# Kernel optimization log

Measured on AMD Instinct MI355X. Metric: run time of the kernel, lower is better.

Reference implementation:

```python
import jax, jax.numpy as jnp
import numpy as np

N_NODES = 50000
N_EDGES = 800000
D = 64


def setup_inputs() -> dict:
    key = jax.random.key(0)
    ks = jax.random.split(key, 5)
    edge_feat = jax.random.normal(ks[0], (N_EDGES, D), dtype=jnp.float32)
    src = jax.random.randint(ks[1], (N_EDGES,), 0, N_NODES, dtype=jnp.int64)
    dst = jax.random.randint(ks[2], (N_EDGES,), 0, N_NODES, dtype=jnp.int64)
    W1 = jax.random.normal(ks[3], (D, D), dtype=jnp.float32) * (1.0 / np.sqrt(D))
    b1 = jnp.zeros((D,), dtype=jnp.float32)
    W2 = jax.random.normal(ks[4], (D, D), dtype=jnp.float32) * (1.0 / np.sqrt(D))
    b2 = jnp.zeros((D,), dtype=jnp.float32)
    return {"edge_feat": edge_feat, "src": src, "dst": dst,
            "W1": W1, "b1": b1, "W2": W2, "b2": b2}


def reference(edge_feat, src, dst, W1, b1, W2, b2):
    # update_all(copy_e, mailbox.sum): node x[v] = sum of edge_feat over edges with dst==v
    node_x = jax.ops.segment_sum(edge_feat, dst, num_segments=N_NODES)  # [N, D]
    # apply_edges: 0.5 * MLP(src.x + dst.x)
    inp = node_x[src] + node_x[dst]                                     # [E, D]
    h = jax.nn.relu(inp @ W1 + b1)
    edge_out = 0.5 * (h @ W2 + b2)                                      # [E, D]
    return edge_out
```

## Files before the change

kernel.cpp:

```cpp
#include <hip/hip_runtime.h>

#define NN 50000
#define NE 800000
#define DD 64
#define NB 196
#define EB 64

__global__ __launch_bounds__(256) void k_hist(const int* __restrict__ dst,
                                              int* __restrict__ cnt) {
    int e = blockIdx.x * 256 + threadIdx.x;
    if (e < NE) atomicAdd(&cnt[dst[e]], 1);
}

__global__ __launch_bounds__(256) void k_block_sum(const int* __restrict__ cnt,
                                                   int* __restrict__ bsum) {
    __shared__ int s[256];
    int i = blockIdx.x * 256 + threadIdx.x;
    s[threadIdx.x] = (i < NN) ? cnt[i] : 0;
    __syncthreads();
    for (int o = 128; o > 0; o >>= 1) {
        if (threadIdx.x < o) s[threadIdx.x] += s[threadIdx.x + o];
        __syncthreads();
    }
    if (threadIdx.x == 0) bsum[blockIdx.x] = s[0];
}

__global__ __launch_bounds__(256) void k_scan_bsum(int* __restrict__ bsum) {
    __shared__ int s[256];
    int t = threadIdx.x;
    int v = (t < NB) ? bsum[t] : 0;
    s[t] = v;
    __syncthreads();
    for (int o = 1; o < 256; o <<= 1) {
        int x = (t >= o) ? s[t - o] : 0;
        __syncthreads();
        s[t] += x;
        __syncthreads();
    }
    if (t < NB) bsum[t] = s[t] - v;
}

__global__ __launch_bounds__(256) void k_scan_final(const int* __restrict__ cnt,
                                                    const int* __restrict__ bsum,
                                                    int* __restrict__ row_start,
                                                    int* __restrict__ cursor) {
    __shared__ int s[256];
    int t = threadIdx.x;
    int i = blockIdx.x * 256 + t;
    int v = (i < NN) ? cnt[i] : 0;
    s[t] = v;
    __syncthreads();
    for (int o = 1; o < 256; o <<= 1) {
        int x = (t >= o) ? s[t - o] : 0;
        __syncthreads();
        s[t] += x;
        __syncthreads();
    }
    int excl = s[t] - v + bsum[blockIdx.x];
    if (i < NN) {
        row_start[i] = excl;
        cursor[i]    = excl;
        if (i == NN - 1) row_start[NN] = excl + v;
    }
}

__global__ __launch_bounds__(256) void k_reorder(const int* __restrict__ dst,
                                                 int* __restrict__ cursor,
                                                 int* __restrict__ eid) {
    int e = blockIdx.x * 256 + threadIdx.x;
    if (e < NE) {
        int pos = atomicAdd(&cursor[dst[e]], 1);
        eid[pos] = e;
    }
}

__global__ __launch_bounds__(256) void k_gather(const float* __restrict__ ef,
                                                const int* __restrict__ row_start,
                                                const int* __restrict__ eid,
                                                float* __restrict__ nx) {
    int lane = threadIdx.x & 63;
    int n = blockIdx.x * 4 + (threadIdx.x >> 6);
    if (n >= NN) return;
    int beg = row_start[n], end = row_start[n + 1];
    float a0 = 0.f, a1 = 0.f, a2 = 0.f, a3 = 0.f;
    int i = beg;
    for (; i + 3 < end; i += 4) {
        int e0 = eid[i], e1 = eid[i + 1], e2 = eid[i + 2], e3 = eid[i + 3];
        a0 += ef[(long)e0 * DD + lane];
        a1 += ef[(long)e1 * DD + lane];
        a2 += ef[(long)e2 * DD + lane];
        a3 += ef[(long)e3 * DD + lane];
    }
    for (; i < end; ++i) {
        a0 += ef[(long)eid[i] * DD + lane];
    }
    nx[(long)n * DD + lane] = (a0 + a1) + (a2 + a3);
}

#define ZERO4 make_float4(0.f, 0.f, 0.f, 0.f)

#define OP16(hv, wv)                                              \
    C0.x = fmaf(hv.x, wv.x, C0.x); C0.y = fmaf(hv.x, wv.y, C0.y); \
    C0.z = fmaf(hv.x, wv.z, C0.z); C0.w = fmaf(hv.x, wv.w, C0.w); \
    C1.x = fmaf(hv.y, wv.x, C1.x); C1.y = fmaf(hv.y, wv.y, C1.y); \
    C1.z = fmaf(hv.y, wv.z, C1.z); C1.w = fmaf(hv.y, wv.w, C1.w); \
    C2.x = fmaf(hv.z, wv.x, C2.x); C2.y = fmaf(hv.z, wv.y, C2.y); \
    C2.z = fmaf(hv.z, wv.z, C2.z); C2.w = fmaf(hv.z, wv.w, C2.w); \
    C3.x = fmaf(hv.w, wv.x, C3.x); C3.y = fmaf(hv.w, wv.y, C3.y); \
    C3.z = fmaf(hv.w, wv.z, C3.z); C3.w = fmaf(hv.w, wv.w, C3.w);

__global__ __launch_bounds__(256, 4) void k_node_mlp(const float* __restrict__ nx,
                                                     const float* __restrict__ W1,
                                                     float* __restrict__ hp) {
    __shared__ float sXT[DD][EB];
    __shared__ float4 sW[DD * DD / 4];
    const float4* Wv = (const float4*)W1;
#pragma unroll
    for (int i = 0; i < 4; ++i)
        sW[threadIdx.x + 256 * i] = Wv[threadIdx.x + 256 * i];

    int lane = threadIdx.x & 63;
    int w    = threadIdx.x >> 6;
    long n   = (long)blockIdx.x * EB + lane;
    const float4* px = (const float4*)(nx + n * DD) + 4 * w;
#pragma unroll
    for (int i = 0; i < 4; ++i) {
        float4 a = (n < NN) ? px[i] : ZERO4;
        int k = 16 * w + 4 * i;
        sXT[k + 0][lane] = a.x;
        sXT[k + 1][lane] = a.y;
        sXT[k + 2][lane] = a.z;
        sXT[k + 3][lane] = a.w;
    }
    __syncthreads();

    int tx = threadIdx.x & 15, ty = threadIdx.x >> 4;
    float4 C0 = ZERO4, C1 = ZERO4, C2 = ZERO4, C3 = ZERO4;
#pragma unroll 4
    for (int k = 0; k < DD; ++k) {
        float4 hv = *(const float4*)&sXT[k][4 * ty];
        float4 wv = sW[k * 16 + tx];
        OP16(hv, wv)
    }
    long r0 = (long)blockIdx.x * EB + 4 * ty;
    if (r0 + 0 < NN) ((float4*)(hp + (r0 + 0) * DD))[tx] = C0;
    if (r0 + 1 < NN) ((float4*)(hp + (r0 + 1) * DD))[tx] = C1;
    if (r0 + 2 < NN) ((float4*)(hp + (r0 + 2) * DD))[tx] = C2;
    if (r0 + 3 < NN) ((float4*)(hp + (r0 + 3) * DD))[tx] = C3;
}

__global__ __launch_bounds__(256, 4) void k_edge_mlp(const float* __restrict__ hp,
                                                     const int* __restrict__ src,
                                                     const int* __restrict__ dst,
                                                     const float* __restrict__ b1,
                                                     const float* __restrict__ W2,
                                                     const float* __restrict__ b2,
                                                     float* __restrict__ out) {
    __shared__ float sHT[DD][EB];
    __shared__ float4 sW[DD * DD / 4];
    const float4* Wv = (const float4*)W2;
#pragma unroll
    for (int i = 0; i < 4; ++i)
        sW[threadIdx.x + 256 * i] = Wv[threadIdx.x + 256 * i];

    int lane = threadIdx.x & 63;
    int w    = threadIdx.x >> 6;
    long e   = (long)blockIdx.x * EB + lane;
    int s = src[e], d = dst[e];
    const float4* ps = (const float4*)(hp + (long)s * DD) + 4 * w;
    const float4* pd = (const float4*)(hp + (long)d * DD) + 4 * w;
    const float4* pb = (const float4*)b1 + 4 * w;
#pragma unroll
    for (int i = 0; i < 4; ++i) {
        float4 a = ps[i], b = pd[i], bb = pb[i];
        int k = 16 * w + 4 * i;
        sHT[k + 0][lane] = fmaxf(a.x + b.x + bb.x, 0.f);
        sHT[k + 1][lane] = fmaxf(a.y + b.y + bb.y, 0.f);
        sHT[k + 2][lane] = fmaxf(a.z + b.z + bb.z, 0.f);
        sHT[k + 3][lane] = fmaxf(a.w + b.w + bb.w, 0.f);
    }
    __syncthreads();

    int tx = threadIdx.x & 15, ty = threadIdx.x >> 4;
    float4 C0 = ZERO4, C1 = ZERO4, C2 = ZERO4, C3 = ZERO4;
#pragma unroll 4
    for (int k = 0; k < DD; ++k) {
        float4 hv = *(const float4*)&sHT[k][4 * ty];
        float4 wv = sW[k * 16 + tx];
        OP16(hv, wv)
    }
    float4 bq = ((const float4*)b2)[tx];
    long r0 = (long)blockIdx.x * EB + 4 * ty;
#define EPI(i, C)                                                   \
    {                                                               \
        float4 r;                                                   \
        r.x = 0.5f * (C.x + bq.x); r.y = 0.5f * (C.y + bq.y);       \
        r.z = 0.5f * (C.z + bq.z); r.w = 0.5f * (C.w + bq.w);       \
        ((float4*)(out + (r0 + i) * DD))[tx] = r;                   \
    }
    EPI(0, C0) EPI(1, C1) EPI(2, C2) EPI(3, C3)
#undef EPI
}

extern "C" void kernel_launch(void* const* d_in, const int* in_sizes, int n_in,
                              void* d_out, int out_size, void* d_ws, size_t ws_size,
                              hipStream_t stream) {
    const float* edge_feat = (const float*)d_in[0];
    const int*   src       = (const int*)d_in[1];
    const int*   dst       = (const int*)d_in[2];
    const float* W1        = (const float*)d_in[3];
    const float* b1        = (const float*)d_in[4];
    const float* W2        = (const float*)d_in[5];
    const float* b2        = (const float*)d_in[6];
    float* out = (float*)d_out;

    char* ws = (char*)d_ws;
    size_t off = 0;
    float* node_x = (float*)(ws + off); off += (size_t)NN * DD * 4;
    float* h_pre  = (float*)(ws + off); off += (size_t)NN * DD * 4;
    int* cnt       = (int*)(ws + off); off += (size_t)NN * 4;
    int* row_start = (int*)(ws + off); off += (size_t)(NN + 1) * 4;
    int* cursor    = (int*)(ws + off); off += (size_t)NN * 4;
    int* bsum      = (int*)(ws + off); off += 256 * 4;
    int* eid       = (int*)(ws + off); off += (size_t)NE * 4;

    hipMemsetAsync(cnt, 0, (size_t)NN * 4, stream);
    k_hist<<<(NE + 255) / 256, 256, 0, stream>>>(dst, cnt);
    k_block_sum<<<NB, 256, 0, stream>>>(cnt, bsum);
    k_scan_bsum<<<1, 256, 0, stream>>>(bsum);
    k_scan_final<<<NB, 256, 0, stream>>>(cnt, bsum, row_start, cursor);
    k_reorder<<<(NE + 255) / 256, 256, 0, stream>>>(dst, cursor, eid);
    k_gather<<<(NN + 3) / 4, 256, 0, stream>>>(edge_feat, row_start, eid, node_x);
    k_node_mlp<<<(NN + EB - 1) / EB, 256, 0, stream>>>(node_x, W1, h_pre);
    k_edge_mlp<<<NE / EB, 256, 0, stream>>>(h_pre, src, dst, b1, W2, b2, out);
}
```

Before: 556.5 us.

## Record atomic ranks in histogram, fuse bsum scan, widen gather unroll, raise occupancy

The histogram kernel now stores each edge's atomic rank, so the placement pass computes its slot as row_start plus rank and needs no second atomic pass or cursor array. The single-block scan of block sums is folded into the final scan kernel, which drops one launch. The gather loop is unrolled to eight independent accumulators for more memory-level parallelism, and the MLP kernels' launch bounds rise to 5 waves per SIMD. In exchange it adds an 800K-int rank array with its extra write and read traffic, and the tighter launch bounds may cause register spills.

Result: faster. 517.3 us (-7.0%).

```diff
diff --git a/kernel.cpp b/kernel.cpp
--- a/kernel.cpp
+++ b/kernel.cpp
@@ -6,10 +6,11 @@
 #define NB 196
 #define EB 64
 
-__global__ __launch_bounds__(256) void k_hist(const int* __restrict__ dst,
-                                              int* __restrict__ cnt) {
+__global__ __launch_bounds__(256) void k_build(const int* __restrict__ dst,
+                                               int* __restrict__ cnt,
+                                               int* __restrict__ rank) {
     int e = blockIdx.x * 256 + threadIdx.x;
-    if (e < NE) atomicAdd(&cnt[dst[e]], 1);
+    if (e < NE) rank[e] = atomicAdd(&cnt[dst[e]], 1);
 }
 
 __global__ __launch_bounds__(256) void k_block_sum(const int* __restrict__ cnt,
@@ -25,27 +26,21 @@
     if (threadIdx.x == 0) bsum[blockIdx.x] = s[0];
 }
 
-__global__ __launch_bounds__(256) void k_scan_bsum(int* __restrict__ bsum) {
+__global__ __launch_bounds__(256) void k_scan_final(const int* __restrict__ cnt,
+                                                    const int* __restrict__ bsum,
+                                                    int* __restrict__ row_start) {
+    __shared__ int sb[256];
     __shared__ int s[256];
     int t = threadIdx.x;
-    int v = (t < NB) ? bsum[t] : 0;
-    s[t] = v;
+    sb[t] = (t < NB) ? bsum[t] : 0;
     __syncthreads();
     for (int o = 1; o < 256; o <<= 1) {
-        int x = (t >= o) ? s[t - o] : 0;
-        __syncthreads();
-        s[t] += x;
-        __syncthreads();
-    }
-    if (t < NB) bsum[t] = s[t] - v;
-}
-
-__global__ __launch_bounds__(256) void k_scan_final(const int* __restrict__ cnt,
-                                                    const int* __restrict__ bsum,
-                                                    int* __restrict__ row_start,
-                                                    int* __restrict__ cursor) {
-    __shared__ int s[256];
-    int t = threadIdx.x;
+        int x = (t >= o) ? sb[t - o] : 0;
+        __syncthreads();
+        sb[t] += x;
+        __syncthreads();
+    }
+    int boff = (blockIdx.x == 0) ? 0 : sb[blockIdx.x - 1];
     int i = blockIdx.x * 256 + t;
     int v = (i < NN) ? cnt[i] : 0;
     s[t] = v;
@@ -56,22 +51,19 @@
         s[t] += x;
         __syncthreads();
     }
-    int excl = s[t] - v + bsum[blockIdx.x];
+    int excl = s[t] - v + boff;
     if (i < NN) {
         row_start[i] = excl;
-        cursor[i]    = excl;
         if (i == NN - 1) row_start[NN] = excl + v;
     }
 }
 
-__global__ __launch_bounds__(256) void k_reorder(const int* __restrict__ dst,
-                                                 int* __restrict__ cursor,
-                                                 int* __restrict__ eid) {
+__global__ __launch_bounds__(256) void k_place(const int* __restrict__ dst,
+                                               const int* __restrict__ rank,
+                                               const int* __restrict__ row_start,
+                                               int* __restrict__ eid) {
     int e = blockIdx.x * 256 + threadIdx.x;
-    if (e < NE) {
-        int pos = atomicAdd(&cursor[dst[e]], 1);
-        eid[pos] = e;
-    }
+    if (e < NE) eid[row_start[dst[e]] + rank[e]] = e;
 }
 
 __global__ __launch_bounds__(256) void k_gather(const float* __restrict__ ef,
@@ -83,18 +75,24 @@
     if (n >= NN) return;
     int beg = row_start[n], end = row_start[n + 1];
     float a0 = 0.f, a1 = 0.f, a2 = 0.f, a3 = 0.f;
+    float a4 = 0.f, a5 = 0.f, a6 = 0.f, a7 = 0.f;
     int i = beg;
-    for (; i + 3 < end; i += 4) {
-        int e0 = eid[i], e1 = eid[i + 1], e2 = eid[i + 2], e3 = eid[i + 3];
+    for (; i + 7 < end; i += 8) {
+        int e0 = eid[i],     e1 = eid[i + 1], e2 = eid[i + 2], e3 = eid[i + 3];
+        int e4 = eid[i + 4], e5 = eid[i + 5], e6 = eid[i + 6], e7 = eid[i + 7];
         a0 += ef[(long)e0 * DD + lane];
         a1 += ef[(long)e1 * DD + lane];
         a2 += ef[(long)e2 * DD + lane];
         a3 += ef[(long)e3 * DD + lane];
+        a4 += ef[(long)e4 * DD + lane];
+        a5 += ef[(long)e5 * DD + lane];
+        a6 += ef[(long)e6 * DD + lane];
+        a7 += ef[(long)e7 * DD + lane];
     }
     for (; i < end; ++i) {
         a0 += ef[(long)eid[i] * DD + lane];
     }
-    nx[(long)n * DD + lane] = (a0 + a1) + (a2 + a3);
+    nx[(long)n * DD + lane] = ((a0 + a1) + (a2 + a3)) + ((a4 + a5) + (a6 + a7));
 }
 
 #define ZERO4 make_float4(0.f, 0.f, 0.f, 0.f)
@@ -109,7 +107,7 @@
     C3.x = fmaf(hv.w, wv.x, C3.x); C3.y = fmaf(hv.w, wv.y, C3.y); \
     C3.z = fmaf(hv.w, wv.z, C3.z); C3.w = fmaf(hv.w, wv.w, C3.w);
 
-__global__ __launch_bounds__(256, 4) void k_node_mlp(const float* __restrict__ nx,
+__global__ __launch_bounds__(256, 5) void k_node_mlp(const float* __restrict__ nx,
                                                      const float* __restrict__ W1,
                                                      float* __restrict__ hp) {
     __shared__ float sXT[DD][EB];
@@ -149,7 +147,7 @@
     if (r0 + 3 < NN) ((float4*)(hp + (r0 + 3) * DD))[tx] = C3;
 }
 
-__global__ __launch_bounds__(256, 4) void k_edge_mlp(const float* __restrict__ hp,
+__global__ __launch_bounds__(256, 5) void k_edge_mlp(const float* __restrict__ hp,
                                                      const int* __restrict__ src,
                                                      const int* __restrict__ dst,
                                                      const float* __restrict__ b1,
@@ -220,16 +218,15 @@
     float* h_pre  = (float*)(ws + off); off += (size_t)NN * DD * 4;
     int* cnt       = (int*)(ws + off); off += (size_t)NN * 4;
     int* row_start = (int*)(ws + off); off += (size_t)(NN + 1) * 4;
-    int* cursor    = (int*)(ws + off); off += (size_t)NN * 4;
     int* bsum      = (int*)(ws + off); off += 256 * 4;
+    int* rank      = (int*)(ws + off); off += (size_t)NE * 4;
     int* eid       = (int*)(ws + off); off += (size_t)NE * 4;
 
     hipMemsetAsync(cnt, 0, (size_t)NN * 4, stream);
-    k_hist<<<(NE + 255) / 256, 256, 0, stream>>>(dst, cnt);
+    k_build<<<(NE + 255) / 256, 256, 0, stream>>>(dst, cnt, rank);
     k_block_sum<<<NB, 256, 0, stream>>>(cnt, bsum);
-    k_scan_bsum<<<1, 256, 0, stream>>>(bsum);
-    k_scan_final<<<NB, 256, 0, stream>>>(cnt, bsum, row_start, cursor);
-    k_reorder<<<(NE + 255) / 256, 256, 0, stream>>>(dst, cursor, eid);
+    k_scan_final<<<NB, 256, 0, stream>>>(cnt, bsum, row_start);
+    k_place<<<(NE + 255) / 256, 256, 0, stream>>>(dst, rank, row_start, eid);
     k_gather<<<(NN + 3) / 4, 256, 0, stream>>>(edge_feat, row_start, eid, node_x);
     k_node_mlp<<<(NN + EB - 1) / EB, 256, 0, stream>>>(node_x, W1, h_pre);
     k_edge_mlp<<<NE / EB, 256, 0, stream>>>(h_pre, src, dst, b1, W2, b2, out);
```
